# Performance work log

Hardware: AMD Instinct MI355X
Metric: run time of the kernel (lower is better)

Reference implementation:

```python
import jax, jax.numpy as jnp
import numpy as np

N = 10000
NFEAT = 256
NHEAD = 4


def setup_inputs() -> dict:
    key = jax.random.key(0)
    k1, k2, k3, k4, k5 = jax.random.split(key, 5)
    stdv = 1.0 / (NFEAT ** 0.5)
    return {
        "adj": jax.random.uniform(k1, (N, N), dtype=jnp.float32),
        "features": jax.random.normal(k2, (N, NFEAT), dtype=jnp.float32),
        "W": jax.random.uniform(k3, (NFEAT, NFEAT), jnp.float32, -stdv, stdv),
        "b": jax.random.uniform(k4, (NFEAT,), jnp.float32, -stdv, stdv),
        "a": jax.random.uniform(k5, (NHEAD, NFEAT, 1), jnp.float32, -stdv, stdv),
    }


def reference(adj, features, W, b, a):
    # --- Laplacian build ---
    deg = adj.sum(axis=1)                              # [N]
    # torch: diag(deg)**-0.5 with inf (off-diag zeros & zero-degree) set to 0
    dinv = jnp.where(deg > 0, deg ** -0.5, 0.0)        # [N]
    # per-head attention: softmax over a size-1 last dim (== ones), kept faithful
    scores = jnp.einsum('nf,hfo->hno', features, a)    # [H, N, 1]
    scores = jax.nn.softmax(scores, axis=2)            # size-1 softmax -> ones
    att = scores.mean(axis=0)[:, 0]                    # [N]
    # D_hat @ (A + diag(att) + I) @ D_hat via diagonal broadcasting (same math)
    M = adj + jnp.diag(att + 1.0)                      # [N, N]
    L = dinv[:, None] * M * dinv[None, :]              # [N, N]
    # --- GCN layer ---
    support = features @ W                             # [N, nhid]
    out = L @ support + b                              # [N, nhid]
    return jax.nn.relu(out)                            # dropout: eval mode (no-op)
```

## Files before the change

### kernel.cpp

```cpp
#include <hip/hip_runtime.h>
#include <hip/hip_bf16.h>
#include <stdint.h>

#define NN 10000
#define NF 256
#define NSTEPS 313
#define NSP 8

typedef float f32x4 __attribute__((ext_vector_type(4)));
typedef __bf16 bf16x8 __attribute__((ext_vector_type(8)));
typedef unsigned short u16;

__device__ __forceinline__ u16 f2bf(float f) {
    __bf16 h = (__bf16)f;
    return __builtin_bit_cast(u16, h);
}

__global__ __launch_bounds__(256) void k_deg(const float* __restrict__ adj,
                                             float* __restrict__ dinv) {
    const int row = blockIdx.x;
    const f32x4* rp = reinterpret_cast<const f32x4*>(adj + (size_t)row * NN);
    float s = 0.f;
    for (int j = threadIdx.x; j < NN / 4; j += 256) {
        f32x4 v = rp[j];
        s += (v[0] + v[1]) + (v[2] + v[3]);
    }
#pragma unroll
    for (int off = 32; off > 0; off >>= 1) s += __shfl_down(s, off, 64);
    __shared__ float red[4];
    const int lane = threadIdx.x & 63, w = threadIdx.x >> 6;
    if (lane == 0) red[w] = s;
    __syncthreads();
    if (threadIdx.x == 0) {
        float deg = (red[0] + red[1]) + (red[2] + red[3]);
        dinv[row] = deg > 0.f ? 1.0f / sqrtf(deg) : 0.0f;
    }
}

__global__ __launch_bounds__(256) void k_support(const float* __restrict__ feat,
                                                 const float* __restrict__ W,
                                                 const float* __restrict__ dinv,
                                                 const float* __restrict__ bias,
                                                 u16* __restrict__ SPT,
                                                 float* __restrict__ accbuf) {
    const int j0 = blockIdx.x * 64;
    const int c0 = blockIdx.y * 64;
    __shared__ float flds[128][64];
    const int t = threadIdx.x;
    const int rg = t & 15, cg = t >> 4;
    const int sr = t >> 2, sf = (t & 3) * 32;
    float acc[4][4] = {};

    for (int half = 0; half < 2; ++half) {
        __syncthreads();
        const int gj = j0 + sr;
#pragma unroll
        for (int i = 0; i < 8; ++i) {
            f32x4 v = {};
            if (gj < NN)
                v = *reinterpret_cast<const f32x4*>(&feat[(size_t)gj * NF + half * 128 + sf + i * 4]);
#pragma unroll
            for (int u = 0; u < 4; ++u) flds[sf + i * 4 + u][sr] = v[u];
        }
        __syncthreads();
#pragma unroll 4
        for (int f = 0; f < 128; ++f) {
            f32x4 fv = *reinterpret_cast<const f32x4*>(&flds[f][rg * 4]);
            f32x4 wv = *reinterpret_cast<const f32x4*>(&W[(size_t)(half * 128 + f) * NF + c0 + cg * 4]);
#pragma unroll
            for (int r = 0; r < 4; ++r)
#pragma unroll
                for (int c = 0; c < 4; ++c)
                    acc[r][c] = fmaf(fv[r], wv[c], acc[r][c]);
        }
    }

    const int jb = j0 + rg * 4;
    if (jb < NN) {
        const f32x4 bv = *reinterpret_cast<const f32x4*>(&bias[c0 + cg * 4]);
        u16 bits[4][4];
#pragma unroll
        for (int r = 0; r < 4; ++r) {
            const float dv = dinv[jb + r];
            f32x4 init;
#pragma unroll
            for (int c = 0; c < 4; ++c) {
                const float sp = acc[r][c] * dv;
                bits[r][c] = f2bf(sp);
                init[c] = 2.f * dv * sp + bv[c];
            }
            *reinterpret_cast<f32x4*>(&accbuf[(size_t)(jb + r) * NF + c0 + cg * 4]) = init;
        }
#pragma unroll
        for (int c = 0; c < 4; ++c) {
            ushort4 v; v.x = bits[0][c]; v.y = bits[1][c]; v.z = bits[2][c]; v.w = bits[3][c];
            *reinterpret_cast<ushort4*>(&SPT[(size_t)(c0 + cg * 4 + c) * NN + jb]) = v;
        }
    }
}

__global__ __launch_bounds__(256, 3) void k_gemm(const float* __restrict__ adj,
                                                 const u16* __restrict__ SPT,
                                                 const float* __restrict__ dinv,
                                                 float* __restrict__ accbuf) {
    const int mt = blockIdx.x, nt = blockIdx.y, ks = blockIdx.z;
    const int t = threadIdx.x;
    const int lane = t & 63, w = t >> 6;
    const int lrow = lane & 15, lk = lane >> 4;
    const int row0 = mt * 256 + w * 64;
    const int n0 = nt * 64;

    const int base = NSTEPS / NSP, extra = NSTEPS % NSP;
    const int s0 = ks * base + (ks < extra ? ks : extra);
    const int s1 = s0 + base + (ks < extra ? 1 : 0);

    const u16* bbase = SPT + (size_t)(n0 + lrow) * NN + lk * 8;

    f32x4 acc[4][4] = {};
    const bf16x8 zz = (bf16x8)(__bf16)0.0f;

    for (int s = s0; s < s1; ++s) {
        const int k0 = s * 32;
        const bool kv = (k0 + lk * 8) < NN;
        const int ka = kv ? (k0 + lk * 8) : 0;
        const int kb = kv ? k0 : 0;

        f32x4 a0[4], a1[4];
#pragma unroll
        for (int i = 0; i < 4; ++i) {
            const int row = row0 + i * 16 + lrow;
            const float* ap = adj + (size_t)(row < NN ? row : 0) * NN + ka;
            a0[i] = *reinterpret_cast<const f32x4*>(ap);
            a1[i] = *reinterpret_cast<const f32x4*>(ap + 4);
        }
        uint4 bq[4];
#pragma unroll
        for (int nf = 0; nf < 4; ++nf)
            bq[nf] = *reinterpret_cast<const uint4*>(bbase + (size_t)nf * 16 * NN + kb);

        bf16x8 af[4], bf[4];
#pragma unroll
        for (int i = 0; i < 4; ++i) {
            bf16x8 a;
            a[0] = (__bf16)a0[i][0]; a[1] = (__bf16)a0[i][1];
            a[2] = (__bf16)a0[i][2]; a[3] = (__bf16)a0[i][3];
            a[4] = (__bf16)a1[i][0]; a[5] = (__bf16)a1[i][1];
            a[6] = (__bf16)a1[i][2]; a[7] = (__bf16)a1[i][3];
            af[i] = kv ? a : zz;
            bf[i] = kv ? *reinterpret_cast<const bf16x8*>(&bq[i]) : zz;
        }
#pragma unroll
        for (int i = 0; i < 4; ++i)
#pragma unroll
            for (int j = 0; j < 4; ++j)
                acc[i][j] = __builtin_amdgcn_mfma_f32_16x16x32_bf16(af[i], bf[j], acc[i][j], 0, 0, 0);
    }

#pragma unroll
    for (int i = 0; i < 4; ++i) {
        const int rb = row0 + i * 16 + lk * 4;
#pragma unroll
        for (int r = 0; r < 4; ++r) {
            const int row = rb + r;
            if (row < NN) {
                const float dv = dinv[row];
#pragma unroll
                for (int j = 0; j < 4; ++j)
                    unsafeAtomicAdd(&accbuf[(size_t)row * NF + n0 + j * 16 + lrow],
                                    dv * acc[i][j][r]);
            }
        }
    }
}

__global__ __launch_bounds__(256) void k_relu(const float* __restrict__ accbuf,
                                              float* __restrict__ out) {
    const int stride = gridDim.x * 256;
    for (int e = blockIdx.x * 256 + threadIdx.x; e < NN * NF / 4; e += stride) {
        f32x4 v = reinterpret_cast<const f32x4*>(accbuf)[e];
        f32x4 o;
#pragma unroll
        for (int c = 0; c < 4; ++c) o[c] = fmaxf(v[c], 0.f);
        reinterpret_cast<f32x4*>(out)[e] = o;
    }
}

extern "C" void kernel_launch(void* const* d_in, const int* in_sizes, int n_in,
                              void* d_out, int out_size, void* d_ws, size_t ws_size,
                              hipStream_t stream) {
    const float* adj  = (const float*)d_in[0];
    const float* feat = (const float*)d_in[1];
    const float* W    = (const float*)d_in[2];
    const float* bias = (const float*)d_in[3];

    char* ws = (char*)d_ws;
    const size_t SPT_OFF  = 0;
    const size_t DINV_OFF = 5120000;
    const size_t ACC_OFF  = 5160192;
    u16*   SPT    = (u16*)(ws + SPT_OFF);
    float* dinv   = (float*)(ws + DINV_OFF);
    float* accbuf = (float*)(ws + ACC_OFF);

    k_deg<<<NN, 256, 0, stream>>>(adj, dinv);
    k_support<<<dim3(157, 4), 256, 0, stream>>>(feat, W, dinv, bias, SPT, accbuf);
    k_gemm<<<dim3(40, 4, NSP), 256, 0, stream>>>(adj, SPT, dinv, accbuf);
    k_relu<<<2048, 256, 0, stream>>>(accbuf, (float*)d_out);
}
```

Measured before the change: 372.5 us.

## Stage adj tiles through LDS with async triple-buffered loads and retile gemm

The adjacency GEMM now stages each 64x32 fp32 tile of adj into a triple-buffered LDS ring using global_load_lds direct loads, with an XOR swizzle and explicit vmcnt waits plus barriers. The block tiling changes from 256 rows x 64 cols to 64 rows x all 256 columns (one wave per 64-col slice), so each adj tile is read once and shared by all four waves. The B operand is register double-buffered. This is meant to hide global load latency and cut redundant adj reads across column tiles. In exchange it adds LDS traffic, a barrier every step, and a larger grid of smaller row tiles.

```diff
diff --git a/kernel.cpp b/kernel.cpp
--- a/kernel.cpp
+++ b/kernel.cpp
@@ -6,6 +6,7 @@
 #define NF 256
 #define NSTEPS 313
 #define NSP 8
+#define DEPTH 3
 
 typedef float f32x4 __attribute__((ext_vector_type(4)));
 typedef __bf16 bf16x8 __attribute__((ext_vector_type(8)));
@@ -103,62 +104,95 @@
                                                  const u16* __restrict__ SPT,
                                                  const float* __restrict__ dinv,
                                                  float* __restrict__ accbuf) {
-    const int mt = blockIdx.x, nt = blockIdx.y, ks = blockIdx.z;
+    const int bid = blockIdx.x;
+    const int ks = bid & 7, mt = bid >> 3;
+    const int m0 = mt * 64;
     const int t = threadIdx.x;
     const int lane = t & 63, w = t >> 6;
+    const int n0 = w * 64;
     const int lrow = lane & 15, lk = lane >> 4;
-    const int row0 = mt * 256 + w * 64;
-    const int n0 = nt * 64;
 
     const int base = NSTEPS / NSP, extra = NSTEPS % NSP;
     const int s0 = ks * base + (ks < extra ? ks : extra);
     const int s1 = s0 + base + (ks < extra ? 1 : 0);
 
+    __shared__ __align__(16) float Abuf[DEPTH][2048];
+
+    auto stage = [&](int d, int s) {
+#pragma unroll
+        for (int is = 0; is < 2; ++is) {
+            const int r = (t >> 3) + is * 32;
+            const int g = (t & 7) ^ (r & 7);
+            const int row = m0 + r;
+            const int kc = s * 32 + g * 4;
+            const float* src = (row < NN && kc < NN) ? (adj + (size_t)row * NN + kc) : adj;
+            __builtin_amdgcn_global_load_lds(
+                (const __attribute__((address_space(1))) void*)src,
+                (__attribute__((address_space(3))) void*)&Abuf[d][t * 4 + is * 1024],
+                16, 0, 0);
+        }
+    };
+
     const u16* bbase = SPT + (size_t)(n0 + lrow) * NN + lk * 8;
+    auto loadB = [&](int s, uint4* bq) {
+        const int k0 = s * 32;
+        const int kb = ((k0 + lk * 8) < NN) ? k0 : 0;
+#pragma unroll
+        for (int nf = 0; nf < 4; ++nf)
+            bq[nf] = *reinterpret_cast<const uint4*>(bbase + (size_t)nf * 16 * NN + kb);
+    };
 
     f32x4 acc[4][4] = {};
-    const bf16x8 zz = (bf16x8)(__bf16)0.0f;
-
+    uint4 bc[4], bn[4];
+
+    loadB(s0, bc);
+    stage(0, s0);
+    if (s0 + 1 < s1) stage(1, s0 + 1);
+
+    int d_cur = 0;
     for (int s = s0; s < s1; ++s) {
+        if (s < s1 - 1) asm volatile("s_waitcnt vmcnt(2)" ::: "memory");
+        else            asm volatile("s_waitcnt vmcnt(0)" ::: "memory");
+        __builtin_amdgcn_s_barrier();
+
+        if (s + 1 < s1) loadB(s + 1, bn);
+        const int d_stage = (d_cur + 2 >= DEPTH) ? d_cur + 2 - DEPTH : d_cur + 2;
+        if (s + 2 < s1) stage(d_stage, s + 2);
+
         const int k0 = s * 32;
         const bool kv = (k0 + lk * 8) < NN;
-        const int ka = kv ? (k0 + lk * 8) : 0;
-        const int kb = kv ? k0 : 0;
-
-        f32x4 a0[4], a1[4];
-#pragma unroll
-        for (int i = 0; i < 4; ++i) {
-            const int row = row0 + i * 16 + lrow;
-            const float* ap = adj + (size_t)(row < NN ? row : 0) * NN + ka;
-            a0[i] = *reinterpret_cast<const f32x4*>(ap);
-            a1[i] = *reinterpret_cast<const f32x4*>(ap + 4);
-        }
-        uint4 bq[4];
-#pragma unroll
-        for (int nf = 0; nf < 4; ++nf)
-            bq[nf] = *reinterpret_cast<const uint4*>(bbase + (size_t)nf * 16 * NN + kb);
-
+        const float* ab = Abuf[d_cur];
+        const bf16x8 zz = (bf16x8)(__bf16)0.0f;
         bf16x8 af[4], bf[4];
 #pragma unroll
-        for (int i = 0; i < 4; ++i) {
+        for (int fi = 0; fi < 4; ++fi) {
+            const int r = fi * 16 + lrow;
+            const int sl0 = (lk * 2) ^ (r & 7);
+            const int sl1 = (lk * 2 + 1) ^ (r & 7);
+            f32x4 x0 = *reinterpret_cast<const f32x4*>(&ab[r * 32 + sl0 * 4]);
+            f32x4 x1 = *reinterpret_cast<const f32x4*>(&ab[r * 32 + sl1 * 4]);
             bf16x8 a;
-            a[0] = (__bf16)a0[i][0]; a[1] = (__bf16)a0[i][1];
-            a[2] = (__bf16)a0[i][2]; a[3] = (__bf16)a0[i][3];
-            a[4] = (__bf16)a1[i][0]; a[5] = (__bf16)a1[i][1];
-            a[6] = (__bf16)a1[i][2]; a[7] = (__bf16)a1[i][3];
-            af[i] = kv ? a : zz;
-            bf[i] = kv ? *reinterpret_cast<const bf16x8*>(&bq[i]) : zz;
+            a[0] = (__bf16)x0[0]; a[1] = (__bf16)x0[1];
+            a[2] = (__bf16)x0[2]; a[3] = (__bf16)x0[3];
+            a[4] = (__bf16)x1[0]; a[5] = (__bf16)x1[1];
+            a[6] = (__bf16)x1[2]; a[7] = (__bf16)x1[3];
+            af[fi] = kv ? a : zz;
+            bf[fi] = kv ? *reinterpret_cast<const bf16x8*>(&bc[fi]) : zz;
         }
 #pragma unroll
         for (int i = 0; i < 4; ++i)
 #pragma unroll
             for (int j = 0; j < 4; ++j)
                 acc[i][j] = __builtin_amdgcn_mfma_f32_16x16x32_bf16(af[i], bf[j], acc[i][j], 0, 0, 0);
+
+#pragma unroll
+        for (int nf = 0; nf < 4; ++nf) bc[nf] = bn[nf];
+        d_cur = (d_cur + 1 == DEPTH) ? 0 : d_cur + 1;
     }
 
 #pragma unroll
     for (int i = 0; i < 4; ++i) {
-        const int rb = row0 + i * 16 + lk * 4;
+        const int rb = m0 + i * 16 + lk * 4;
 #pragma unroll
         for (int r = 0; r < 4; ++r) {
             const int row = rb + r;
@@ -203,6 +237,6 @@
 
     k_deg<<<NN, 256, 0, stream>>>(adj, dinv);
     k_support<<<dim3(157, 4), 256, 0, stream>>>(feat, W, dinv, bias, SPT, accbuf);
-    k_gemm<<<dim3(40, 4, NSP), 256, 0, stream>>>(adj, SPT, dinv, accbuf);
+    k_gemm<<<157 * NSP, 256, 0, stream>>>(adj, SPT, dinv, accbuf);
     k_relu<<<2048, 256, 0, stream>>>(accbuf, (float*)d_out);
 }
```

New measurement: 302.8 us. -18.7%, faster.
